# Kernel optimization log

Hardware: AMD Instinct MI355X
Metric: run time of the kernel (lower is better)

Reference implementation:

```python
import jax, jax.numpy as jnp
import numpy as np

N = 100000      # nodes
E = 800000      # edges
F_IN = 128      # input feature dim
HID = 8         # per-head hidden
HEADS = 8
HD = HID * HEADS  # 64
G = 128         # graphs in batch
C = 10          # classes
SLOPE = 0.2     # leaky relu negative slope


def setup_inputs() -> dict:
    key = jax.random.key(0)
    ks = iter(jax.random.split(key, 48))
    def rn(shape, scale=0.1):
        return jax.random.normal(next(ks), shape, jnp.float32) * scale
    inp = {
        'x': jax.random.normal(next(ks), (N, F_IN), jnp.float32),
        'edge_index': jax.random.randint(next(ks), (2, E), 0, N),
        'batch': jnp.sort(jax.random.randint(next(ks), (N,), 0, G)),
        # GAT layer 1
        'W1': rn((F_IN, HEADS * HID)), 'as1': rn((HEADS, HID)), 'ad1': rn((HEADS, HID)), 'b1': jnp.zeros((HEADS * HID,), jnp.float32),
        # GAT layer 2
        'W2': rn((HD, HEADS * HID)), 'as2': rn((HEADS, HID)), 'ad2': rn((HEADS, HID)), 'b2': jnp.zeros((HEADS * HID,), jnp.float32),
        # node attention MLP (HD -> HD//2 -> 2)
        'na_w1': rn((HD, HD // 2)), 'na_b1': jnp.zeros((HD // 2,), jnp.float32), 'na_w2': rn((HD // 2, 2)), 'na_b2': jnp.zeros((2,), jnp.float32),
        # edge attention MLP (2*HD -> HD -> 2)
        'ea_w1': rn((2 * HD, HD)), 'ea_b1': jnp.zeros((HD,), jnp.float32), 'ea_w2': rn((HD, 2)), 'ea_b2': jnp.zeros((2,), jnp.float32),
        # GCN causal / trivial
        'gc_w': rn((HD, HD)), 'gc_b': jnp.zeros((HD,), jnp.float32),
        'gt_w': rn((HD, HD)), 'gt_b': jnp.zeros((HD,), jnp.float32),
        # readouts
        'rc_w': rn((HD, HD)), 'rc_b': jnp.zeros((HD,), jnp.float32),
        'rt_w': rn((HD, HD)), 'rt_b': jnp.zeros((HD,), jnp.float32),
        # classifiers (HD -> HD//2 -> C), combined (2HD -> HD -> C)
        'cc_w1': rn((HD, HD // 2)), 'cc_b1': jnp.zeros((HD // 2,), jnp.float32), 'cc_w2': rn((HD // 2, C)), 'cc_b2': jnp.zeros((C,), jnp.float32),
        'ct_w1': rn((HD, HD // 2)), 'ct_b1': jnp.zeros((HD // 2,), jnp.float32), 'ct_w2': rn((HD // 2, C)), 'ct_b2': jnp.zeros((C,), jnp.float32),
        'cm_w1': rn((2 * HD, HD)), 'cm_b1': jnp.zeros((HD,), jnp.float32), 'cm_w2': rn((HD, C)), 'cm_b2': jnp.zeros((C,), jnp.float32),
    }
    return inp


def _mlp2(h, w1, b1, w2, b2):
    return jax.nn.relu(h @ w1 + b1) @ w2 + b2


def reference(x, edge_index, batch,
              W1, as1, ad1, b1, W2, as2, ad2, b2,
              na_w1, na_b1, na_w2, na_b2,
              ea_w1, ea_b1, ea_w2, ea_b2,
              gc_w, gc_b, gt_w, gt_b,
              rc_w, rc_b, rt_w, rt_b,
              cc_w1, cc_b1, cc_w2, cc_b2,
              ct_w1, ct_b1, ct_w2, ct_b2,
              cm_w1, cm_b1, cm_w2, cm_b2):
    src, dst = edge_index[0], edge_index[1]
    loop = jnp.arange(N)
    s2 = jnp.concatenate([src, loop])  # edges + self-loops (PyG GATConv/GCNConv add self-loops)
    d2 = jnp.concatenate([dst, loop])

    def gat(h_in, W, a_s, a_d, b):
        h = (h_in @ W).reshape(N, HEADS, HID)
        es = jnp.einsum('nhd,hd->nh', h, a_s)
        ed = jnp.einsum('nhd,hd->nh', h, a_d)
        logit = jax.nn.leaky_relu(es[s2] + ed[d2], SLOPE)      # [E+N, H]
        m = jax.ops.segment_max(logit, d2, num_segments=N)
        ex = jnp.exp(logit - m[d2])
        den = jax.ops.segment_sum(ex, d2, num_segments=N)
        alpha = ex / (den[d2] + 1e-16)
        out = jax.ops.segment_sum(h[s2] * alpha[..., None], d2, num_segments=N)
        return out.reshape(N, HEADS * HID) + b

    # GNN encoder (dropout disabled: eval mode)
    H1 = jax.nn.elu(gat(x, W1, as1, ad1, b1))
    H = gat(H1, W2, as2, ad2, b2)                              # [N, HD]

    # node attention
    na = jax.nn.softmax(_mlp2(H, na_w1, na_b1, na_w2, na_b2), axis=1)
    alpha_c, alpha_t = na[:, 0], na[:, 1]
    # edge attention (original edges, no self-loops)
    ef = jnp.concatenate([H[src], H[dst]], axis=1)             # [E, 2*HD]
    ea = jax.nn.softmax(_mlp2(ef, ea_w1, ea_b1, ea_w2, ea_b2), axis=1)
    beta_c, beta_t = ea[:, 0], ea[:, 1]

    Hc = H * alpha_c[:, None]
    Ht = H * alpha_t[:, None]

    def gcn(h_in, w, b, ew):
        # PyG gcn_norm: self-loops with weight 1, symmetric deg^-1/2 normalization
        w_full = jnp.concatenate([ew, jnp.ones((N,), h_in.dtype)])
        deg = jax.ops.segment_sum(w_full, d2, num_segments=N)
        dis = jnp.where(deg > 0, jax.lax.rsqrt(jnp.maximum(deg, 1e-20)), 0.0)
        norm = dis[s2] * w_full * dis[d2]
        h = h_in @ w
        return jax.ops.segment_sum(h[s2] * norm[:, None], d2, num_segments=N) + b

    Gc = gcn(Hc, gc_w, gc_b, beta_c)
    Gt = gcn(Ht, gt_w, gt_b, beta_t)

    # readout: linear then global_add_pool
    hGc = jax.ops.segment_sum(Gc @ rc_w + rc_b, batch, num_segments=G)  # [G, HD]
    hGt = jax.ops.segment_sum(Gt @ rt_w + rt_b, batch, num_segments=G)

    zc = _mlp2(hGc, cc_w1, cc_b1, cc_w2, cc_b2)
    zt = _mlp2(hGt, ct_w1, ct_b1, ct_w2, ct_b2)
    # RandomIntervention: within-graph node shuffle followed by add-pool == plain add-pool
    h_comb = jnp.concatenate([hGc + hGt], axis=1) if False else (hGc + hGt)
    zp = _mlp2(jnp.concatenate([h_comb, jnp.zeros_like(h_comb)], axis=1), cm_w1, cm_b1, cm_w2, cm_b2) if False else _mlp2_comb(h_comb, cm_w1, cm_b1, cm_w2, cm_b2)
    return (zc, zt, zp, hGc, hGt)


def _mlp2_comb(h_comb, cm_w1, cm_b1, cm_w2, cm_b2):
    # original: classifier_combined takes hidden_dim*2 input; forward feeds h_G_c + shuffled_h_G_t
    # which is [G, HD]; to match Linear(2*HD, ...) we use the first HD rows of cm_w1 twice?
    # NO -- the original code as written passes a [G, HD] tensor to a Linear(2*HD, HD) layer,
    # which would error in torch. Faithful runnable interpretation: combined feature is
    # concat([h_G_c, shuffled_h_G_t]) of width 2*HD (the standard CAL formulation).
    return jax.nn.relu(h_comb @ cm_w1 + cm_b1) @ cm_w2 + cm_b2


# clean final definition overriding the commented exploration above
def reference(x, edge_index, batch,
              W1, as1, ad1, b1, W2, as2, ad2, b2,
              na_w1, na_b1, na_w2, na_b2,
              ea_w1, ea_b1, ea_w2, ea_b2,
              gc_w, gc_b, gt_w, gt_b,
              rc_w, rc_b, rt_w, rt_b,
              cc_w1, cc_b1, cc_w2, cc_b2,
              ct_w1, ct_b1, ct_w2, ct_b2,
              cm_w1, cm_b1, cm_w2, cm_b2):
    src, dst = edge_index[0], edge_index[1]
    loop = jnp.arange(N)
    s2 = jnp.concatenate([src, loop])
    d2 = jnp.concatenate([dst, loop])

    def gat(h_in, W, a_s, a_d, b):
        h = (h_in @ W).reshape(N, HEADS, HID)
        es = jnp.einsum('nhd,hd->nh', h, a_s)
        ed = jnp.einsum('nhd,hd->nh', h, a_d)
        logit = jax.nn.leaky_relu(es[s2] + ed[d2], SLOPE)
        m = jax.ops.segment_max(logit, d2, num_segments=N)
        ex = jnp.exp(logit - m[d2])
        den = jax.ops.segment_sum(ex, d2, num_segments=N)
        alpha = ex / (den[d2] + 1e-16)
        out = jax.ops.segment_sum(h[s2] * alpha[..., None], d2, num_segments=N)
        return out.reshape(N, HEADS * HID) + b

    H1 = jax.nn.elu(gat(x, W1, as1, ad1, b1))
    H = gat(H1, W2, as2, ad2, b2)

    na = jax.nn.softmax(_mlp2(H, na_w1, na_b1, na_w2, na_b2), axis=1)
    alpha_c, alpha_t = na[:, 0], na[:, 1]
    ef = jnp.concatenate([H[src], H[dst]], axis=1)
    ea = jax.nn.softmax(_mlp2(ef, ea_w1, ea_b1, ea_w2, ea_b2), axis=1)
    beta_c, beta_t = ea[:, 0], ea[:, 1]

    Hc = H * alpha_c[:, None]
    Ht = H * alpha_t[:, None]

    def gcn(h_in, w, b, ew):
        w_full = jnp.concatenate([ew, jnp.ones((N,), h_in.dtype)])
        deg = jax.ops.segment_sum(w_full, d2, num_segments=N)
        dis = jnp.where(deg > 0, jax.lax.rsqrt(jnp.maximum(deg, 1e-20)), 0.0)
        norm = dis[s2] * w_full * dis[d2]
        h = h_in @ w
        return jax.ops.segment_sum(h[s2] * norm[:, None], d2, num_segments=N) + b

    Gc = gcn(Hc, gc_w, gc_b, beta_c)
    Gt = gcn(Ht, gt_w, gt_b, beta_t)

    hGc = jax.ops.segment_sum(Gc @ rc_w + rc_b, batch, num_segments=G)
    hGt = jax.ops.segment_sum(Gt @ rt_w + rt_b, batch, num_segments=G)

    zc = _mlp2(hGc, cc_w1, cc_b1, cc_w2, cc_b2)
    zt = _mlp2(hGt, ct_w1, ct_b1, ct_w2, ct_b2)
    # RandomIntervention with sorted batch: within-graph permutation + add-pool == add-pool
    h_comb = jnp.concatenate([hGc, hGt], axis=1)  # [G, 2*HD] for Linear(2*HD, ...)
    zp = _mlp2(h_comb, cm_w1, cm_b1, cm_w2, cm_b2)
    return (zc, zt, zp, hGc, hGt)


if __name__ == '__main__':
    out = reference(**setup_inputs())
    print([o.shape for o in out])
```

## Files before the change

kernel.cpp:

```cpp
#include <hip/hip_runtime.h>
#include <hip/hip_bf16.h>

#define N_NODES 100000
#define E_EDGES 800000
#define E2 (E_EDGES + N_NODES)
#define FIN 128
#define HD 64
#define NH 8
#define NG 128
#define NC 10
#define SLOPE 0.2f
#define SELF_FLAG 0x40000000
#define SRC_MASK  0x3FFFFFFF
#define NSCAN_BLK 391
#define NBLK64 1563
#define GB 16

#define U1_STRIPES 261
#define U1_GRID (2 + U1_STRIPES * 7)
#define U1_HISTB (U1_STRIPES * 4)
#define T1 (U1_STRIPES * 3)
#define U2_STRIPES 391
#define U2_GRID (U2_STRIPES * 11)

// ... 65 lines not shown
#pragma unroll 2
        for (int k = 0; k < KH; k += 4) {
            float4 w0 = Wsv[(k + 0) * 16 + tc];
            float4 w1 = Wsv[(k + 1) * 16 + tc];
            float4 w2 = Wsv[(k + 2) * 16 + tc];
            float4 w3 = Wsv[(k + 3) * 16 + tc];
            int kq = (h * KH + k) >> 2;
#pragma unroll
            for (int i = 0; i < 4; ++i) {
                float4 r = R4[(tr * 4 + i) * (RS / 4) + kq];
                acc[i][0] = fmaf(r.x, w0.x, fmaf(r.y, w1.x, fmaf(r.z, w2.x, fmaf(r.w, w3.x, acc[i][0]))));
                acc[i][1] = fmaf(r.x, w0.y, fmaf(r.y, w1.y, fmaf(r.z, w2.y, fmaf(r.w, w3.y, acc[i][1]))));
                acc[i][2] = fmaf(r.x, w0.z, fmaf(r.y, w1.z, fmaf(r.z, w2.z, fmaf(r.w, w3.z, acc[i][2]))));
                acc[i][3] = fmaf(r.x, w0.w, fmaf(r.y, w1.w, fmaf(r.z, w2.w, fmaf(r.w, w3.w, acc[i][3]))));
            }
        }
    }

    int j0 = tc * 4;
#pragma unroll
    for (int i = 0; i < 4; ++i) {
        int n = base + tr * 4 + i;
        if (n < N_NODES) {
            ushort4 ov;
            ov.x = f2bf(acc[i][0]); ov.y = f2bf(acc[i][1]);
            ov.z = f2bf(acc[i][2]); ov.w = f2bf(acc[i][3]);
            *(ushort4*)(outB + (size_t)n * 64 + j0) = ov;
        }
    }
    if (MODE == 1) {
        float s0[4], s1[4];
#pragma unroll
        for (int i = 0; i < 4; ++i) {
            float pes = 0.f, ped = 0.f;
#pragma unroll
            for (int q = 0; q < 4; ++q) {
                pes = fmaf(acc[i][q], a_s[j0 + q], pes);
                ped = fmaf(acc[i][q], a_d[j0 + q], ped);
            }
            pes += __shfl_xor(pes, 1, 64);
            ped += __shfl_xor(ped, 1, 64);
            s0[i] = pes; s1[i] = ped;
        }
        if ((tc & 1) == 0) {
            int h = tc >> 1;
#pragma unroll
            for (int i = 0; i < 4; ++i) {
                int n = base + tr * 4 + i;
                if (n < N_NODES) {
                    es[n * NH + h] = s0[i];
                    ed[n * NH + h] = s1[i];
                }
            }
        }
    }
}

__device__ __forceinline__
void gemm_dual_body(float* smem, int tile,
                    const bfu* __restrict__ in, const float* __restrict__ W0,
                    const float* __restrict__ W1,
                    bfu* __restrict__ out0, bfu* __restrict__ out1)
{
    float* Ws   = smem;
    float* rows = smem + 8192;
    int t = threadIdx.x;
    int base = tile * 64;
    {
        const float4* W0v = (const float4*)W0;
        const float4* W1v = (const float4*)W1;
        float4* Wsv = (float4*)Ws;
        for (int i = t; i < 1024; i += 256) { Wsv[i] = W0v[i]; Wsv[1024 + i] = W1v[i]; }
    }
    for (int i = t; i < 64 * 8; i += 256) {
        int r = i >> 3, c = (i & 7) * 8;
        int n = base + r;
        uint4 v = make_uint4(0, 0, 0, 0);
        if (n < N_NODES) v = *(const uint4*)(in + (size_t)n * 64 + c);
        float* dp = rows + r * 68 + c;
        *(float4*)dp       = make_float4(bflo(v.x), bfhi(v.x), bflo(v.y), bfhi(v.y));
        *(float4*)(dp + 4) = make_float4(bflo(v.z), bfhi(v.z), bflo(v.w), bfhi(v.w));
    }
    __syncthreads();
    int tr = t >> 4, tc = t & 15;
    float a0[4][4] = {}, a1[4][4] = {};
    const float4* Wsv = (const float4*)Ws;
    const float4* R4 = (const float4*)rows;
#pragma unroll 2
    for (int k = 0; k < 64; k += 4) {
        float4 p0 = Wsv[(k + 0) * 16 + tc];
        float4 p1 = Wsv[(k + 1) * 16 + tc];
        float4 p2 = Wsv[(k + 2) * 16 + tc];
        float4 p3 = Wsv[(k + 3) * 16 + tc];
        float4 q0 = Wsv[1024 + (k + 0) * 16 + tc];
        float4 q1 = Wsv[1024 + (k + 1) * 16 + tc];
        float4 q2 = Wsv[1024 + (k + 2) * 16 + tc];
        float4 q3 = Wsv[1024 + (k + 3) * 16 + tc];
        int kq = k >> 2;
#pragma unroll
        for (int i = 0; i < 4; ++i) {
            float4 r = R4[(tr * 4 + i) * 17 + kq];
            a0[i][0] = fmaf(r.x, p0.x, fmaf(r.y, p1.x, fmaf(r.z, p2.x, fmaf(r.w, p3.x, a0[i][0]))));
            a0[i][1] = fmaf(r.x, p0.y, fmaf(r.y, p1.y, fmaf(r.z, p2.y, fmaf(r.w, p3.y, a0[i][1]))));
            a0[i][2] = fmaf(r.x, p0.z, fmaf(r.y, p1.z, fmaf(r.z, p2.z, fmaf(r.w, p3.z, a0[i][2]))));
            a0[i][3] = fmaf(r.x, p0.w, fmaf(r.y, p1.w, fmaf(r.z, p2.w, fmaf(r.w, p3.w, a0[i][3]))));
            a1[i][0] = fmaf(r.x, q0.x, fmaf(r.y, q1.x, fmaf(r.z, q2.x, fmaf(r.w, q3.x, a1[i][0]))));
            a1[i][1] = fmaf(r.x, q0.y, fmaf(r.y, q1.y, fmaf(r.z, q2.y, fmaf(r.w, q3.y, a1[i][1]))));
            a1[i][2] = fmaf(r.x, q0.z, fmaf(r.y, q1.z, fmaf(r.z, q2.z, fmaf(r.w, q3.z, a1[i][2]))));
            a1[i][3] = fmaf(r.x, q0.w, fmaf(r.y, q1.w, fmaf(r.z, q2.w, fmaf(r.w, q3.w, a1[i][3]))));
        }
    }
    int j0 = tc * 4;
#pragma unroll
    for (int i = 0; i < 4; ++i) {
        int n = base + tr * 4 + i;
        if (n >= N_NODES) continue;
        ushort4 o0, o1;
        o0.x = f2bf(a0[i][0]); o0.y = f2bf(a0[i][1]);
        o0.z = f2bf(a0[i][2]); o0.w = f2bf(a0[i][3]);
        o1.x = f2bf(a1[i][0]); o1.y = f2bf(a1[i][1]);
        o1.z = f2bf(a1[i][2]); o1.w = f2bf(a1[i][3]);
        *(ushort4*)(out0 + (size_t)n * 64 + j0) = o0;
        *(ushort4*)(out1 + (size_t)n * 64 + j0) = o1;
    }
}

__device__ __forceinline__
void node_att_body(float* smem, int tile,
                   const bfu* __restrict__ H, const float* __restrict__ w1,
                   const float* __restrict__ b1, const float* __restrict__ w2,
                   const float* __restrict__ b2, float2* __restrict__ al2)
{
    float* w1s  = smem;
    float* w2s  = smem + 2048;
    float* rows = smem + 2112;
    int t = threadIdx.x;
    int base = tile * 64;
    {
        const float4* w1v = (const float4*)w1;
        float4* dst = (float4*)w1s;
        for (int i = t; i < 512; i += 256) dst[i] = w1v[i];
    }
    if (t < 64) w2s[t] = w2[t];
    for (int i = t; i < 64 * 8; i += 256) {
        int r = i >> 3, c = (i & 7) * 8;
        int n = base + r;
        uint4 v = make_uint4(0, 0, 0, 0);
        if (n < N_NODES) v = *(const uint4*)(H + (size_t)n * 64 + c);
        float* dp = rows + r * 65 + c;
        dp[0] = bflo(v.x); dp[1] = bfhi(v.x);
        dp[2] = bflo(v.y); dp[3] = bfhi(v.y);
        dp[4] = bflo(v.z); dp[5] = bfhi(v.z);
        dp[6] = bflo(v.w); dp[7] = bfhi(v.w);
    }
    __syncthreads();
    int tr = t >> 3;
    int tc = t & 7;
    float4 bv = *(const float4*)(b1 + tc * 4);
    float4 acc0 = bv, acc1 = bv;
    const float4* w1sv = (const float4*)w1s;
#pragma unroll 8
    for (int k = 0; k < 64; ++k) {
        float4 w = w1sv[k * 8 + tc];
        float r0 = rows[tr * 65 + k];
        float r1 = rows[(tr + 32) * 65 + k];
        acc0.x = fmaf(r0, w.x, acc0.x); acc0.y = fmaf(r0, w.y, acc0.y);
        acc0.z = fmaf(r0, w.z, acc0.z); acc0.w = fmaf(r0, w.w, acc0.w);
        acc1.x = fmaf(r1, w.x, acc1.x); acc1.y = fmaf(r1, w.y, acc1.y);
        acc1.z = fmaf(r1, w.z, acc1.z); acc1.w = fmaf(r1, w.w, acc1.w);
    }
    float z00 = 0.f, z01 = 0.f, z10 = 0.f, z11 = 0.f;
    float h0, w20, w21;
    int j0 = tc * 4;
#pragma unroll
    for (int q = 0; q < 4; ++q) {
        float a0q = q == 0 ? acc0.x : q == 1 ? acc0.y : q == 2 ? acc0.z : acc0.w;
        float a1q = q == 0 ? acc1.x : q == 1 ? acc1.y : q == 2 ? acc1.z : acc1.w;
        w20 = w2s[(j0 + q) * 2]; w21 = w2s[(j0 + q) * 2 + 1];
        h0 = fmaxf(a0q, 0.f);
        z00 = fmaf(h0, w20, z00); z01 = fmaf(h0, w21, z01);
        h0 = fmaxf(a1q, 0.f);
        z10 = fmaf(h0, w20, z10); z11 = fmaf(h0, w21, z11);
    }
#pragma unroll
    for (int o = 1; o < 8; o <<= 1) {
        z00 += __shfl_xor(z00, o, 64); z01 += __shfl_xor(z01, o, 64);
        z10 += __shfl_xor(z10, o, 64); z11 += __shfl_xor(z11, o, 64);
    }
    if (tc == 0) {
        int n0 = base + tr, n1 = base + tr + 32;
        if (n0 < N_NODES) {
            float zz0 = z00 + b2[0], zz1 = z01 + b2[1];
            float mx = fmaxf(zz0, zz1);
            float e0 = __expf(zz0 - mx), e1 = __expf(zz1 - mx);
            float ss = e0 + e1;
            al2[n0] = make_float2(e0 / ss, e1 / ss);
        }
        if (n1 < N_NODES) {
            float zz0 = z10 + b2[0], zz1 = z11 + b2[1];
            float mx = fmaxf(zz0, zz1);
            float e0 = __expf(zz0 - mx), e1 = __expf(zz1 - mx);
            float ss = e0 + e1;
            al2[n1] = make_float2(e0 / ss, e1 / ss);
        }
    }
}

__device__ __forceinline__
void weight_prep_body(float* smem,
                      const float* __restrict__ gw, const float* __restrict__ gb,
                      const float* __restrict__ rw, const float* __restrict__ rb,
                      float* __restrict__ Wp, float* __restrict__ bp)
{
    float* A = smem;
    float* B = smem + 4096;
    int t = threadIdx.x;
    {
        const float4* ga = (const float4*)gw;
        const float4* rA = (const float4*)rw;
        float4* dA = (float4*)A; float4* dB = (float4*)B;
        for (int i = t; i < 1024; i += 256) { dA[i] = ga[i]; dB[i] = rA[i]; }
    }
    __syncthreads();
    for (int e = t * 16; e < t * 16 + 16; ++e) {
        int k = e >> 6, j = e & 63;
        float acc = 0.f;
#pragma unroll 8
        for (int m = 0; m < 64; ++m) acc = fmaf(A[k * 64 + m], B[m * 64 + j], acc);
        Wp[e] = acc;
    }
    if (t < 64) {
        float acc = rb[t];
#pragma unroll 8
        for (int m = 0; m < 64; ++m) acc = fmaf(gb[m], B[m * 64 + t], acc);
        bp[t] = acc;
    }
}

__global__ __launch_bounds__(256)
void u1_fused(const float* __restrict__ x, const float* __restrict__ W1,
              bfu* __restrict__ B0, const float* __restrict__ as1,
              const float* __restrict__ ad1, float* __restrict__ es,
              float* __restrict__ ed,
              const int* __restrict__ ei, int* __restrict__ cnt,
              int* __restrict__ rank,
              const float* __restrict__ gc_w, const float* __restrict__ gc_b,
              const float* __restrict__ rc_w, const float* __restrict__ rc_b,
              const float* __restrict__ gt_w, const float* __restrict__ gt_b,
              const float* __restrict__ rt_w, const float* __restrict__ rt_b,
              float* __restrict__ Wcp, float* __restrict__ bcp,
              float* __restrict__ Wtp, float* __restrict__ btp)
{
    __shared__ __align__(16) float smem[12544];
    int b = blockIdx.x;
    if (b < 2) {
        if (b == 0) weight_prep_body(smem, gc_w, gc_b, rc_w, rc_b, Wcp, bcp);
        else        weight_prep_body(smem, gt_w, gt_b, rt_w, rt_b, Wtp, btp);
        return;
    }
    int u = b - 2;
    int stripe = u / 7, r = u % 7;
    if (r < 3) {
        gemm_tile_body<float, FIN, 1>(smem, stripe * 3 + r, x, W1, B0, as1, ad1, es, ed);
    } else {
        int idx = stripe * 4 + (r - 3);
        int t = threadIdx.x;
        const int STR = U1_HISTB * 256;
        for (int e = idx * 256 + t; e < E_EDGES; e += 2 * STR) {
            int e1 = e + STR;
            int d0 = ei[E_EDGES + e];
            int r0 = atomicAdd(&cnt[d0], 1);
            int r1 = 0;
            bool has1 = e1 < E_EDGES;
            if (has1) r1 = atomicAdd(&cnt[ei[E_EDGES + e1]], 1);
            rank[e] = r0;
            if (has1) rank[e1] = r1;
        }
    }
}

__global__ __launch_bounds__(256)
void u2_fused(const float* __restrict__ x, const float* __restrict__ W1,
              bfu* __restrict__ B0, const float* __restrict__ as1,
              const float* __restrict__ ad1, float* __restrict__ es,
              float* __restrict__ ed,
              const int* __restrict__ ei, const int* __restrict__ rank,
              const int* __restrict__ offs,
              int* __restrict__ csr, int* __restrict__ csrd)
{
    __shared__ __align__(16) float smem[12544];
    int b = blockIdx.x;
    int stripe = b / 11, r = b % 11;
    int t = threadIdx.x;
    if (r < 8) {
        int e = (stripe * 8 + r) * 256 + t;
        if (e < E_EDGES) {
            int s = ei[e], d = ei[E_EDGES + e];
            csr[offs[d] + rank[e]] = s;
        }
    } else if (r < 10) {
        int tile = T1 + stripe * 2 + (r - 8);
        if (tile < NBLK64)
            gemm_tile_body<float, FIN, 1>(smem, tile, x, W1, B0, as1, ad1, es, ed);
    } else {
        int n = stripe * 256 + t;
        if (n < N_NODES) {
            int pb = offs[n], pe = offs[n + 1];
            for (int p = pb; p < pe; ++p) csrd[p] = n;
            csr[pe - 1] = n | SELF_FLAG;
        }
    }
}

__global__ __launch_bounds__(256)
void u3_fused(const bfu* __restrict__ B2,
              const float* __restrict__ na_w1, const float* __restrict__ na_b1,
              const float* __restrict__ na_w2, const float* __restrict__ na_b2,
              float2* __restrict__ al2,
              const float* __restrict__ ea_w1,
              bfu* __restrict__ P1, bfu* __restrict__ P2)
{
    __shared__ __align__(16) float smem[12544];
    int b = blockIdx.x;
    if (b & 1) node_att_body(smem, b >> 1, B2, na_w1, na_b1, na_w2, na_b2, al2);
    else       gemm_dual_body(smem, b >> 1, B2, ea_w1, ea_w1 + 64 * 64, P1, P2);
}

__global__ __launch_bounds__(256)
void gemm_tile_k64(const bfu* __restrict__ in, const float* __restrict__ W,
                   bfu* __restrict__ outB,
                   const float* __restrict__ a_s, const float* __restrict__ a_d,
                   float* __restrict__ es, float* __restrict__ ed)
{
    __shared__ __align__(16) float smem[64 * 64 + 64 * 68];
    gemm_tile_body<bfu, 64, 1>(smem, blockIdx.x, in, W, outB, a_s, a_d, es, ed);
}

__global__ void csr_scan1(const int* __restrict__ cnt, int* __restrict__ offs,
                          int* __restrict__ bsum, const int* __restrict__ batch,
                          int* __restrict__ glo)
{
    __shared__ int tmp[256];
    int t = threadIdx.x;
    int i = blockIdx.x * 256 + t;
    int v = (i < N_NODES) ? cnt[i] + 1 : 0;
    tmp[t] = v; __syncthreads();
#pragma unroll
    for (int o = 1; o < 256; o <<= 1) {
        int a = (t >= o) ? tmp[t - o] : 0;
        __syncthreads();
        tmp[t] += a;
        __syncthreads();
    }
    if (i < N_NODES) offs[i] = tmp[t] - v;
    if (t == 255) bsum[blockIdx.x] = tmp[255];
    if (blockIdx.x == 0 && t <= NG) {
        int l = 0, r = N_NODES;
        while (l < r) { int m = (l + r) >> 1; if (batch[m] < t) l = m + 1; else r = m; }
        glo[t] = l;
    }
}

__global__ void csr_scan23(int* __restrict__ offs, const int* __restrict__ bsum)
{
    __shared__ int tmp[256];
    int b = blockIdx.x;
    int t = threadIdx.x;
    int s = 0;
    for (int j = t; j < b; j += 256) s += bsum[j];
    tmp[t] = s; __syncthreads();
#pragma unroll
    for (int o = 128; o > 0; o >>= 1) {
        if (t < o) tmp[t] += tmp[t + o];
        __syncthreads();
    }
    int prefix = tmp[0];
    int i = b * 256 + t;
    if (i < N_NODES) offs[i] += prefix;
// ... 25 lines not shown
        float ex0 = __expf(l0);
        float ex1 = __expf(l1);
        den += ex0 + ex1;
        ushort4 ra = *(const ushort4*)(hsrcB + (size_t)s0 * HD + fl * 4);
        ushort4 rb = *(const ushort4*)(hsrcB + (size_t)s1 * HD + fl * 4);
        acc.x = fmaf(bf2f(ra.x), ex0, fmaf(bf2f(rb.x), ex1, acc.x));
        acc.y = fmaf(bf2f(ra.y), ex0, fmaf(bf2f(rb.y), ex1, acc.y));
        acc.z = fmaf(bf2f(ra.z), ex0, fmaf(bf2f(rb.z), ex1, acc.z));
        acc.w = fmaf(bf2f(ra.w), ex0, fmaf(bf2f(rb.w), ex1, acc.w));
    }
    if (p < end) {
        int s = csr[p] & SRC_MASK;
        float l = lrelu(es[s * NH + h] + edv);
        float ex = __expf(l);
        den += ex;
        ushort4 rb = *(const ushort4*)(hsrcB + (size_t)s * HD + fl * 4);
        acc.x = fmaf(bf2f(rb.x), ex, acc.x);
        acc.y = fmaf(bf2f(rb.y), ex, acc.y);
        acc.z = fmaf(bf2f(rb.z), ex, acc.z);
        acc.w = fmaf(bf2f(rb.w), ex, acc.w);
    }
#pragma unroll
    for (int o = 16; o <= 32; o <<= 1) {
        den   += __shfl_xor(den,   o, 64);
        acc.x += __shfl_xor(acc.x, o, 64);
        acc.y += __shfl_xor(acc.y, o, 64);
        acc.z += __shfl_xor(acc.z, o, 64);
        acc.w += __shfl_xor(acc.w, o, 64);
    }
    if (g == 0) {
        float inv = 1.f / (den + 1e-16f);
        float4 bv = *(const float4*)(bias + fl * 4);
        float v0 = acc.x * inv + bv.x;
        float v1 = acc.y * inv + bv.y;
        float v2 = acc.z * inv + bv.z;
        float v3 = acc.w * inv + bv.w;
        if (ELU) {
            v0 = v0 > 0.f ? v0 : (__expf(v0) - 1.f);
            v1 = v1 > 0.f ? v1 : (__expf(v1) - 1.f);
            v2 = v2 > 0.f ? v2 : (__expf(v2) - 1.f);
            v3 = v3 > 0.f ? v3 : (__expf(v3) - 1.f);
        }
        ushort4 ov;
        ov.x = f2bf(v0); ov.y = f2bf(v1); ov.z = f2bf(v2); ov.w = f2bf(v3);
        *(ushort4*)(outB + (size_t)n * HD + fl * 4) = ov;
    }
}

__global__ void edge_att_node(const int* __restrict__ offs, const int* __restrict__ csr,
                              const bfu* __restrict__ P1b, const bfu* __restrict__ P2b,
                              const float* __restrict__ b1, const float* __restrict__ w2,
                              const float* __restrict__ b2,
                              const float2* __restrict__ al2,
                              float2* __restrict__ beta2, float2* __restrict__ dis2,
                              float2* __restrict__ prod2)
{
    int n = blockIdx.x * 4 + (threadIdx.x >> 6);
    int lane = threadIdx.x & 63;
    if (n >= N_NODES) return;
    int slot = lane >> 3, q = lane & 7;
    uint4 U2 = *(const uint4*)(P2b + (size_t)n * 64 + q * 8);
    const float4* pb = (const float4*)(b1 + q * 8);
    const float4* pw = (const float4*)(w2 + q * 16);
    float4 c0 = pb[0], c1 = pb[1];
    float4 w0 = pw[0], w1v = pw[1], w2v = pw[2], w3v = pw[3];
    float wd0 = w0.x - w0.y,   wd1 = w0.z - w0.w;
    float wd2 = w1v.x - w1v.y, wd3 = w1v.z - w1v.w;
    float wd4 = w2v.x - w2v.y, wd5 = w2v.z - w2v.w;
    float wd6 = w3v.x - w3v.y, wd7 = w3v.z - w3v.w;
    float zbd = b2[0] - b2[1];
    float d0 = bflo(U2.x) + c0.x, d1 = bfhi(U2.x) + c0.y;
    float d2 = bflo(U2.y) + c0.z, d3 = bfhi(U2.y) + c0.w;
    float d4 = bflo(U2.z) + c1.x, d5 = bfhi(U2.z) + c1.y;
    float d6 = bflo(U2.w) + c1.z, d7 = bfhi(U2.w) + c1.w;
    int beg = offs[n], endr = offs[n + 1] - 1;
    float dc = 0.f, dt = 0.f;
    for (int p = beg + slot; p < endr; p += 8) {
        int s = csr[p];
        uint4 U1 = *(const uint4*)(P1b + (size_t)s * 64 + q * 8);
        float h0 = fmaxf(bflo(U1.x) + d0, 0.f);
        float h1 = fmaxf(bfhi(U1.x) + d1, 0.f);
        float h2 = fmaxf(bflo(U1.y) + d2, 0.f);
        float h3 = fmaxf(bfhi(U1.y) + d3, 0.f);
        float h4 = fmaxf(bflo(U1.z) + d4, 0.f);
        float h5 = fmaxf(bfhi(U1.z) + d5, 0.f);
        float h6 = fmaxf(bflo(U1.w) + d6, 0.f);
        float h7 = fmaxf(bfhi(U1.w) + d7, 0.f);
        float z = fmaf(h0, wd0, fmaf(h1, wd1, fmaf(h2, wd2, fmaf(h3, wd3,
                  fmaf(h4, wd4, fmaf(h5, wd5, fmaf(h6, wd6, h7 * wd7)))))));
        z += __shfl_xor(z, 1, 64);
        z += __shfl_xor(z, 2, 64);
        z += __shfl_xor(z, 4, 64);
        if (q == 0) {
            z += zbd;
            float e = __expf(-fabsf(z));
            float inv = 1.f / (1.f + e);
            float bx = z >= 0.f ? inv : e * inv;
            float by = z >= 0.f ? e * inv : inv;
            beta2[p] = make_float2(bx, by);
            dc += bx; dt += by;
        }
    }
    dc += __shfl_xor(dc, 8, 64);  dt += __shfl_xor(dt, 8, 64);
    dc += __shfl_xor(dc, 16, 64); dt += __shfl_xor(dt, 16, 64);
    dc += __shfl_xor(dc, 32, 64); dt += __shfl_xor(dt, 32, 64);
    if (lane == 0) {
        dc += 1.f; dt += 1.f;
        float ic = rsqrtf(fmaxf(dc, 1e-20f));
        float it = rsqrtf(fmaxf(dt, 1e-20f));
        dis2[n] = make_float2(ic, it);
        float2 al = al2[n];
        prod2[n] = make_float2(ic * al.x, it * al.y);
    }
}

__global__ __launch_bounds__(256)
void gcn_readout_fused(const int* __restrict__ offs, const int* __restrict__ csr,
                       const int* __restrict__ csrd, const int* __restrict__ glo,
                       const bfu* __restrict__ HB,
                       const float2* __restrict__ beta2, const float2* __restrict__ dis2,
                       const float2* __restrict__ prod2,
                       float* __restrict__ Pc, float* __restrict__ Pt)
{
    int g = blockIdx.x / GB, b = blockIdx.x % GB;
    int t = threadIdx.x;
    int pbeg = offs[glo[g]], pend = offs[glo[g + 1]];
    int total = pend - pbeg;
    int chunk = (total + GB - 1) / GB;
    int start = pbeg + b * chunk;
    int end = start + chunk;
    if (end > pend) end = pend;
    if (start > pend) start = pend;
    int slot = t >> 4, fl = t & 15;
    float4 a1 = make_float4(0.f, 0.f, 0.f, 0.f);
    float4 a2 = make_float4(0.f, 0.f, 0.f, 0.f);
    int p = start + slot;
    for (; p + 48 < end; p += 64) {
#pragma unroll
        for (int j = 0; j < 4; ++j) {
            int pp = p + j * 16;
            int sv = csr[pp];
            int s = sv & SRC_MASK;
            float2 bb = beta2[pp];
            if (sv & SELF_FLAG) { bb.x = 1.f; bb.y = 1.f; }
            float2 pr = prod2[s];
            float2 dv = dis2[csrd[pp]];
            float wc = pr.x * bb.x * dv.x;
            float wt = pr.y * bb.y * dv.y;
            ushort4 r0 = *(const ushort4*)(HB + (size_t)s * HD + fl * 4);
            float f0 = bf2f(r0.x), f1 = bf2f(r0.y), f2 = bf2f(r0.z), f3 = bf2f(r0.w);
            a1.x = fmaf(f0, wc, a1.x); a1.y = fmaf(f1, wc, a1.y);
            a1.z = fmaf(f2, wc, a1.z); a1.w = fmaf(f3, wc, a1.w);
            a2.x = fmaf(f0, wt, a2.x); a2.y = fmaf(f1, wt, a2.y);
            a2.z = fmaf(f2, wt, a2.z); a2.w = fmaf(f3, wt, a2.w);
        }
    }
    for (; p < end; p += 16) {
        int sv = csr[p];
        int s = sv & SRC_MASK;
        float2 bb = beta2[p];
        if (sv & SELF_FLAG) { bb.x = 1.f; bb.y = 1.f; }
        float2 pr = prod2[s];
        float2 dv = dis2[csrd[p]];
        float wc = pr.x * bb.x * dv.x;
        float wt = pr.y * bb.y * dv.y;
        ushort4 r0 = *(const ushort4*)(HB + (size_t)s * HD + fl * 4);
        float f0 = bf2f(r0.x), f1 = bf2f(r0.y), f2 = bf2f(r0.z), f3 = bf2f(r0.w);
        a1.x = fmaf(f0, wc, a1.x); a1.y = fmaf(f1, wc, a1.y);
        a1.z = fmaf(f2, wc, a1.z); a1.w = fmaf(f3, wc, a1.w);
        a2.x = fmaf(f0, wt, a2.x); a2.y = fmaf(f1, wt, a2.y);
        a2.z = fmaf(f2, wt, a2.z); a2.w = fmaf(f3, wt, a2.w);
    }
    __shared__ float redc[16 * 64], redt[16 * 64];
    *(float4*)(redc + slot * 64 + fl * 4) = a1;
    *(float4*)(redt + slot * 64 + fl * 4) = a2;
    __syncthreads();
    if (t < 64) {
        float sc = 0.f, st = 0.f;
#pragma unroll
        for (int s = 0; s < 16; ++s) { sc += redc[s * 64 + t]; st += redt[s * 64 + t]; }
        Pc[(size_t)blockIdx.x * 64 + t] = sc;
        Pt[(size_t)blockIdx.x * 64 + t] = st;
    }
}

__global__ __launch_bounds__(64)
void head_final(const float* __restrict__ Pc, const float* __restrict__ Pt,
                const int* __restrict__ glo,
                const float* __restrict__ Wcp, const float* __restrict__ bcp,
                const float* __restrict__ Wtp, const float* __restrict__ btp,
                const float* __restrict__ cc_w1, const float* __restrict__ cc_b1,
                const float* __restrict__ cc_w2, const float* __restrict__ cc_b2,
                const float* __restrict__ ct_w1, const float* __restrict__ ct_b1,
                const float* __restrict__ ct_w2, const float* __restrict__ ct_b2,
                const float* __restrict__ cm_w1, const float* __restrict__ cm_b1,
                const float* __restrict__ cm_w2, const float* __restrict__ cm_b2,
                float* __restrict__ out)
{
    int g = blockIdx.x;
    int t = threadIdx.x;
    __shared__ float scl[64], stl[64], hgc[64], hgt[64], hid[64];
    float sc = 0.f, st = 0.f;
#pragma unroll
    for (int b = 0; b < GB; ++b) {
        sc += Pc[(size_t)(g * GB + b) * 64 + t];
        st += Pt[(size_t)(g * GB + b) * 64 + t];
    }
    scl[t] = sc; stl[t] = st;
    float c = (float)(glo[g + 1] - glo[g]);
    __syncthreads();
    {
        float a = c * bcp[t], bb = c * btp[t];
#pragma unroll 8
        for (int k = 0; k < 64; ++k) {
            a  = fmaf(scl[k], Wcp[k * 64 + t], a);
            bb = fmaf(stl[k], Wtp[k * 64 + t], bb);
        }
        hgc[t] = a; hgt[t] = bb;
// ... 49 lines not shown

extern "C" void kernel_launch(void* const* d_in, const int* in_sizes, int n_in,
                              void* d_out, int out_size, void* d_ws, size_t ws_size,
                              hipStream_t stream)
{
    const float* x     = (const float*)d_in[0];
    const int*   ei    = (const int*)d_in[1];
    const int*   batch = (const int*)d_in[2];
    const float* W1    = (const float*)d_in[3];
    const float* as1   = (const float*)d_in[4];
    const float* ad1   = (const float*)d_in[5];
    const float* b1    = (const float*)d_in[6];
    const float* W2    = (const float*)d_in[7];
    const float* as2   = (const float*)d_in[8];
    const float* ad2   = (const float*)d_in[9];
    const float* b2    = (const float*)d_in[10];
    const float* na_w1 = (const float*)d_in[11];
    const float* na_b1 = (const float*)d_in[12];
    const float* na_w2 = (const float*)d_in[13];
    const float* na_b2 = (const float*)d_in[14];
    const float* ea_w1 = (const float*)d_in[15];
    const float* ea_b1 = (const float*)d_in[16];
    const float* ea_w2 = (const float*)d_in[17];
    const float* ea_b2 = (const float*)d_in[18];
    const float* gc_w  = (const float*)d_in[19];
    const float* gc_b  = (const float*)d_in[20];
    const float* gt_w  = (const float*)d_in[21];
    const float* gt_b  = (const float*)d_in[22];
    const float* rc_w  = (const float*)d_in[23];
    const float* rc_b  = (const float*)d_in[24];
    const float* rt_w  = (const float*)d_in[25];
    const float* rt_b  = (const float*)d_in[26];
    const float* cc_w1 = (const float*)d_in[27];
    const float* cc_b1 = (const float*)d_in[28];
    const float* cc_w2 = (const float*)d_in[29];
    const float* cc_b2 = (const float*)d_in[30];
    const float* ct_w1 = (const float*)d_in[31];
    const float* ct_b1 = (const float*)d_in[32];
    const float* ct_w2 = (const float*)d_in[33];
    const float* ct_b2 = (const float*)d_in[34];
    const float* cm_w1 = (const float*)d_in[35];
    const float* cm_b1 = (const float*)d_in[36];
    const float* cm_w2 = (const float*)d_in[37];
    const float* cm_b2 = (const float*)d_in[38];
    float* out = (float*)d_out;

    float* ws = (float*)d_ws;
    size_t o = 0;
    const size_t nf = (size_t)N_NODES * HD;
    float* es    = ws + o; o += (size_t)N_NODES * NH;
    float* ed    = ws + o; o += (size_t)N_NODES * NH;
    float2* al2  = (float2*)(ws + o); o += (size_t)N_NODES * 2;
    float2* beta2= (float2*)(ws + o); o += (size_t)E2 * 2;
    float2* dis2 = (float2*)(ws + o); o += (size_t)N_NODES * 2;
    float2* prod2= (float2*)(ws + o); o += (size_t)N_NODES * 2;
    bfu* B0      = (bfu*)(ws + o); o += nf / 2;
    bfu* B1      = (bfu*)(ws + o); o += nf / 2;
    bfu* B2      = (bfu*)(ws + o); o += nf / 2;
    bfu* BH1     = (bfu*)(ws + o); o += nf / 2;
    int* csr     = (int*)(ws + o); o += E2;
    int* csrd    = (int*)(ws + o); o += E2;
    int* offs    = (int*)(ws + o); o += N_NODES + 1;
    float* Pc    = ws + o; o += (size_t)NG * GB * 64;
    float* Pt    = ws + o; o += (size_t)NG * GB * 64;
    float* Wcp   = ws + o; o += 4096;
    float* Wtp   = ws + o; o += 4096;
    float* bcp   = ws + o; o += 64;
    float* btp   = ws + o; o += 64;
    int* glo     = (int*)(ws + o); o += NG + 2;
    int* cnt  = (int*)beta2;
    int* bsum = (int*)dis2;
    int* rank = (int*)B1;

    const int NW_BLKS = N_NODES / 4;

    hipMemsetAsync(cnt, 0, (size_t)N_NODES * 4, stream);
    u1_fused<<<U1_GRID, 256, 0, stream>>>(x, W1, B0, as1, ad1, es, ed,
                                          ei, cnt, rank,
                                          gc_w, gc_b, rc_w, rc_b,
                                          gt_w, gt_b, rt_w, rt_b,
                                          Wcp, bcp, Wtp, btp);
    csr_scan1<<<NSCAN_BLK, 256, 0, stream>>>(cnt, offs, bsum, batch, glo);
    csr_scan23<<<NSCAN_BLK, 256, 0, stream>>>(offs, bsum);

    u2_fused<<<U2_GRID, 256, 0, stream>>>(x, W1, B0, as1, ad1, es, ed,
                                          ei, rank, offs, csr, csrd);

    gat_aggregate4<1><<<NW_BLKS, 256, 0, stream>>>(offs, csr, es, ed, B0, b1, BH1);

    gemm_tile_k64<<<NBLK64, 256, 0, stream>>>(BH1, W2, B0, as2, ad2, es, ed);
    gat_aggregate4<0><<<NW_BLKS, 256, 0, stream>>>(offs, csr, es, ed, B0, b2, B2);

    u3_fused<<<2 * NBLK64, 256, 0, stream>>>(B2, na_w1, na_b1, na_w2, na_b2, al2,
                                             ea_w1, B0, B1);

    edge_att_node<<<NW_BLKS, 256, 0, stream>>>(offs, csr, B0, B1,
                                               ea_b1, ea_w2, ea_b2, al2,
                                               beta2, dis2, prod2);

    gcn_readout_fused<<<NG * GB, 256, 0, stream>>>(offs, csr, csrd, glo, B2,
                                                   beta2, dis2, prod2, Pc, Pt);

    head_final<<<NG, 64, 0, stream>>>(Pc, Pt, glo,
                                      Wcp, bcp, Wtp, btp,
                                      cc_w1, cc_b1, cc_w2, cc_b2,
                                      ct_w1, ct_b1, ct_w2, ct_b2,
                                      cm_w1, cm_b1, cm_w2, cm_b2, out);
    (void)in_sizes; (void)n_in; (void)out_size; (void)ws_size;
}
```

Before: 479.2 us.

## Fold destination degree norm into edge weights and drop csrd array

```diff
diff --git a/kernel.cpp b/kernel.cpp
--- a/kernel.cpp
+++ b/kernel.cpp
@@ -141,156 +141,6 @@
                     ed[n * NH + h] = s1[i];
                 }
             }
-        }
-    }
-}
-
-__device__ __forceinline__
-void gemm_dual_body(float* smem, int tile,
-                    const bfu* __restrict__ in, const float* __restrict__ W0,
-                    const float* __restrict__ W1,
-                    bfu* __restrict__ out0, bfu* __restrict__ out1)
-{
-    float* Ws   = smem;
-    float* rows = smem + 8192;
-    int t = threadIdx.x;
-    int base = tile * 64;
-    {
-        const float4* W0v = (const float4*)W0;
-        const float4* W1v = (const float4*)W1;
-        float4* Wsv = (float4*)Ws;
-        for (int i = t; i < 1024; i += 256) { Wsv[i] = W0v[i]; Wsv[1024 + i] = W1v[i]; }
-    }
-    for (int i = t; i < 64 * 8; i += 256) {
-        int r = i >> 3, c = (i & 7) * 8;
-        int n = base + r;
-        uint4 v = make_uint4(0, 0, 0, 0);
-        if (n < N_NODES) v = *(const uint4*)(in + (size_t)n * 64 + c);
-        float* dp = rows + r * 68 + c;
-        *(float4*)dp       = make_float4(bflo(v.x), bfhi(v.x), bflo(v.y), bfhi(v.y));
-        *(float4*)(dp + 4) = make_float4(bflo(v.z), bfhi(v.z), bflo(v.w), bfhi(v.w));
-    }
-    __syncthreads();
-    int tr = t >> 4, tc = t & 15;
-    float a0[4][4] = {}, a1[4][4] = {};
-    const float4* Wsv = (const float4*)Ws;
-    const float4* R4 = (const float4*)rows;
-#pragma unroll 2
-    for (int k = 0; k < 64; k += 4) {
-        float4 p0 = Wsv[(k + 0) * 16 + tc];
-        float4 p1 = Wsv[(k + 1) * 16 + tc];
-        float4 p2 = Wsv[(k + 2) * 16 + tc];
-        float4 p3 = Wsv[(k + 3) * 16 + tc];
-        float4 q0 = Wsv[1024 + (k + 0) * 16 + tc];
-        float4 q1 = Wsv[1024 + (k + 1) * 16 + tc];
-        float4 q2 = Wsv[1024 + (k + 2) * 16 + tc];
-        float4 q3 = Wsv[1024 + (k + 3) * 16 + tc];
-        int kq = k >> 2;
-#pragma unroll
-        for (int i = 0; i < 4; ++i) {
-            float4 r = R4[(tr * 4 + i) * 17 + kq];
-            a0[i][0] = fmaf(r.x, p0.x, fmaf(r.y, p1.x, fmaf(r.z, p2.x, fmaf(r.w, p3.x, a0[i][0]))));
-            a0[i][1] = fmaf(r.x, p0.y, fmaf(r.y, p1.y, fmaf(r.z, p2.y, fmaf(r.w, p3.y, a0[i][1]))));
-            a0[i][2] = fmaf(r.x, p0.z, fmaf(r.y, p1.z, fmaf(r.z, p2.z, fmaf(r.w, p3.z, a0[i][2]))));
-            a0[i][3] = fmaf(r.x, p0.w, fmaf(r.y, p1.w, fmaf(r.z, p2.w, fmaf(r.w, p3.w, a0[i][3]))));
-            a1[i][0] = fmaf(r.x, q0.x, fmaf(r.y, q1.x, fmaf(r.z, q2.x, fmaf(r.w, q3.x, a1[i][0]))));
-            a1[i][1] = fmaf(r.x, q0.y, fmaf(r.y, q1.y, fmaf(r.z, q2.y, fmaf(r.w, q3.y, a1[i][1]))));
-            a1[i][2] = fmaf(r.x, q0.z, fmaf(r.y, q1.z, fmaf(r.z, q2.z, fmaf(r.w, q3.z, a1[i][2]))));
-            a1[i][3] = fmaf(r.x, q0.w, fmaf(r.y, q1.w, fmaf(r.z, q2.w, fmaf(r.w, q3.w, a1[i][3]))));
-        }
-    }
-    int j0 = tc * 4;
-#pragma unroll
-    for (int i = 0; i < 4; ++i) {
-        int n = base + tr * 4 + i;
-        if (n >= N_NODES) continue;
-        ushort4 o0, o1;
-        o0.x = f2bf(a0[i][0]); o0.y = f2bf(a0[i][1]);
-        o0.z = f2bf(a0[i][2]); o0.w = f2bf(a0[i][3]);
-        o1.x = f2bf(a1[i][0]); o1.y = f2bf(a1[i][1]);
-        o1.z = f2bf(a1[i][2]); o1.w = f2bf(a1[i][3]);
-        *(ushort4*)(out0 + (size_t)n * 64 + j0) = o0;
-        *(ushort4*)(out1 + (size_t)n * 64 + j0) = o1;
-    }
-}
-
-__device__ __forceinline__
-void node_att_body(float* smem, int tile,
-                   const bfu* __restrict__ H, const float* __restrict__ w1,
-                   const float* __restrict__ b1, const float* __restrict__ w2,
-                   const float* __restrict__ b2, float2* __restrict__ al2)
-{
-    float* w1s  = smem;
-    float* w2s  = smem + 2048;
-    float* rows = smem + 2112;
-    int t = threadIdx.x;
-    int base = tile * 64;
-    {
-        const float4* w1v = (const float4*)w1;
-        float4* dst = (float4*)w1s;
-        for (int i = t; i < 512; i += 256) dst[i] = w1v[i];
-    }
-    if (t < 64) w2s[t] = w2[t];
-    for (int i = t; i < 64 * 8; i += 256) {
-        int r = i >> 3, c = (i & 7) * 8;
-        int n = base + r;
-        uint4 v = make_uint4(0, 0, 0, 0);
-        if (n < N_NODES) v = *(const uint4*)(H + (size_t)n * 64 + c);
-        float* dp = rows + r * 65 + c;
-        dp[0] = bflo(v.x); dp[1] = bfhi(v.x);
-        dp[2] = bflo(v.y); dp[3] = bfhi(v.y);
-        dp[4] = bflo(v.z); dp[5] = bfhi(v.z);
-        dp[6] = bflo(v.w); dp[7] = bfhi(v.w);
-    }
-    __syncthreads();
-    int tr = t >> 3;
-    int tc = t & 7;
-    float4 bv = *(const float4*)(b1 + tc * 4);
-    float4 acc0 = bv, acc1 = bv;
-    const float4* w1sv = (const float4*)w1s;
-#pragma unroll 8
-    for (int k = 0; k < 64; ++k) {
-        float4 w = w1sv[k * 8 + tc];
-        float r0 = rows[tr * 65 + k];
-        float r1 = rows[(tr + 32) * 65 + k];
-        acc0.x = fmaf(r0, w.x, acc0.x); acc0.y = fmaf(r0, w.y, acc0.y);
-        acc0.z = fmaf(r0, w.z, acc0.z); acc0.w = fmaf(r0, w.w, acc0.w);
-        acc1.x = fmaf(r1, w.x, acc1.x); acc1.y = fmaf(r1, w.y, acc1.y);
-        acc1.z = fmaf(r1, w.z, acc1.z); acc1.w = fmaf(r1, w.w, acc1.w);
-    }
-    float z00 = 0.f, z01 = 0.f, z10 = 0.f, z11 = 0.f;
-    float h0, w20, w21;
-    int j0 = tc * 4;
-#pragma unroll
-    for (int q = 0; q < 4; ++q) {
-        float a0q = q == 0 ? acc0.x : q == 1 ? acc0.y : q == 2 ? acc0.z : acc0.w;
-        float a1q = q == 0 ? acc1.x : q == 1 ? acc1.y : q == 2 ? acc1.z : acc1.w;
-        w20 = w2s[(j0 + q) * 2]; w21 = w2s[(j0 + q) * 2 + 1];
-        h0 = fmaxf(a0q, 0.f);
-        z00 = fmaf(h0, w20, z00); z01 = fmaf(h0, w21, z01);
-        h0 = fmaxf(a1q, 0.f);
-        z10 = fmaf(h0, w20, z10); z11 = fmaf(h0, w21, z11);
-    }
-#pragma unroll
-    for (int o = 1; o < 8; o <<= 1) {
-        z00 += __shfl_xor(z00, o, 64); z01 += __shfl_xor(z01, o, 64);
-        z10 += __shfl_xor(z10, o, 64); z11 += __shfl_xor(z11, o, 64);
-    }
-    if (tc == 0) {
-        int n0 = base + tr, n1 = base + tr + 32;
-        if (n0 < N_NODES) {
-            float zz0 = z00 + b2[0], zz1 = z01 + b2[1];
-            float mx = fmaxf(zz0, zz1);
-            float e0 = __expf(zz0 - mx), e1 = __expf(zz1 - mx);
-            float ss = e0 + e1;
-            al2[n0] = make_float2(e0 / ss, e1 / ss);
-        }
-        if (n1 < N_NODES) {
-            float zz0 = z10 + b2[0], zz1 = z11 + b2[1];
-            float mx = fmaxf(zz0, zz1);
-            float e0 = __expf(zz0 - mx), e1 = __expf(zz1 - mx);
-            float ss = e0 + e1;
-            al2[n1] = make_float2(e0 / ss, e1 / ss);
         }
     }
 }
@@ -375,7 +225,7 @@
               float* __restrict__ ed,
               const int* __restrict__ ei, const int* __restrict__ rank,
               const int* __restrict__ offs,
-              int* __restrict__ csr, int* __restrict__ csrd)
+              int* __restrict__ csr)
 {
     __shared__ __align__(16) float smem[12544];
     int b = blockIdx.x;
@@ -394,25 +244,145 @@
     } else {
         int n = stripe * 256 + t;
         if (n < N_NODES) {
-            int pb = offs[n], pe = offs[n + 1];
-            for (int p = pb; p < pe; ++p) csrd[p] = n;
-            csr[pe - 1] = n | SELF_FLAG;
+            csr[offs[n + 1] - 1] = n | SELF_FLAG;
         }
     }
 }
 
 __global__ __launch_bounds__(256)
-void u3_fused(const bfu* __restrict__ B2,
+void u3_fused(const bfu* __restrict__ in,
               const float* __restrict__ na_w1, const float* __restrict__ na_b1,
               const float* __restrict__ na_w2, const float* __restrict__ na_b2,
               float2* __restrict__ al2,
               const float* __restrict__ ea_w1,
-              bfu* __restrict__ P1, bfu* __restrict__ P2)
+              bfu* __restrict__ out0, bfu* __restrict__ out1)
 {
     __shared__ __align__(16) float smem[12544];
-    int b = blockIdx.x;
-    if (b & 1) node_att_body(smem, b >> 1, B2, na_w1, na_b1, na_w2, na_b2, al2);
-    else       gemm_dual_body(smem, b >> 1, B2, ea_w1, ea_w1 + 64 * 64, P1, P2);
+    float* Ws   = smem;
+    float* rows = smem + 8192;
+    int t = threadIdx.x;
+    int base = blockIdx.x * 64;
+    const float* W0 = ea_w1;
+    const float* W1 = ea_w1 + 64 * 64;
+    {
+        const float4* W0v = (const float4*)W0;
+        const float4* W1v = (const float4*)W1;
+        float4* Wsv = (float4*)Ws;
+        for (int i = t; i < 1024; i += 256) { Wsv[i] = W0v[i]; Wsv[1024 + i] = W1v[i]; }
+    }
+    for (int i = t; i < 64 * 8; i += 256) {
+        int r = i >> 3, c = (i & 7) * 8;
+        int n = base + r;
+        uint4 v = make_uint4(0, 0, 0, 0);
+        if (n < N_NODES) v = *(const uint4*)(in + (size_t)n * 64 + c);
+        float* dp = rows + r * 68 + c;
+        *(float4*)dp       = make_float4(bflo(v.x), bfhi(v.x), bflo(v.y), bfhi(v.y));
+        *(float4*)(dp + 4) = make_float4(bflo(v.z), bfhi(v.z), bflo(v.w), bfhi(v.w));
+    }
+    __syncthreads();
+    {
+        int tr = t >> 4, tc = t & 15;
+        float a0[4][4] = {}, a1[4][4] = {};
+        const float4* Wsv = (const float4*)Ws;
+        const float4* R4 = (const float4*)rows;
+#pragma unroll 2
+        for (int k = 0; k < 64; k += 4) {
+            float4 p0 = Wsv[(k + 0) * 16 + tc];
+            float4 p1 = Wsv[(k + 1) * 16 + tc];
+            float4 p2 = Wsv[(k + 2) * 16 + tc];
+            float4 p3 = Wsv[(k + 3) * 16 + tc];
+            float4 q0 = Wsv[1024 + (k + 0) * 16 + tc];
+            float4 q1 = Wsv[1024 + (k + 1) * 16 + tc];
+            float4 q2 = Wsv[1024 + (k + 2) * 16 + tc];
+            float4 q3 = Wsv[1024 + (k + 3) * 16 + tc];
+            int kq = k >> 2;
+#pragma unroll
+            for (int i = 0; i < 4; ++i) {
+                float4 r = R4[(tr * 4 + i) * 17 + kq];
+                a0[i][0] = fmaf(r.x, p0.x, fmaf(r.y, p1.x, fmaf(r.z, p2.x, fmaf(r.w, p3.x, a0[i][0]))));
+                a0[i][1] = fmaf(r.x, p0.y, fmaf(r.y, p1.y, fmaf(r.z, p2.y, fmaf(r.w, p3.y, a0[i][1]))));
+                a0[i][2] = fmaf(r.x, p0.z, fmaf(r.y, p1.z, fmaf(r.z, p2.z, fmaf(r.w, p3.z, a0[i][2]))));
+                a0[i][3] = fmaf(r.x, p0.w, fmaf(r.y, p1.w, fmaf(r.z, p2.w, fmaf(r.w, p3.w, a0[i][3]))));
+                a1[i][0] = fmaf(r.x, q0.x, fmaf(r.y, q1.x, fmaf(r.z, q2.x, fmaf(r.w, q3.x, a1[i][0]))));
+                a1[i][1] = fmaf(r.x, q0.y, fmaf(r.y, q1.y, fmaf(r.z, q2.y, fmaf(r.w, q3.y, a1[i][1]))));
+                a1[i][2] = fmaf(r.x, q0.z, fmaf(r.y, q1.z, fmaf(r.z, q2.z, fmaf(r.w, q3.z, a1[i][2]))));
+                a1[i][3] = fmaf(r.x, q0.w, fmaf(r.y, q1.w, fmaf(r.z, q2.w, fmaf(r.w, q3.w, a1[i][3]))));
+            }
+        }
+        int j0 = tc * 4;
+#pragma unroll
+        for (int i = 0; i < 4; ++i) {
+            int n = base + tr * 4 + i;
+            if (n >= N_NODES) continue;
+            ushort4 o0, o1;
+            o0.x = f2bf(a0[i][0]); o0.y = f2bf(a0[i][1]);
+            o0.z = f2bf(a0[i][2]); o0.w = f2bf(a0[i][3]);
+            o1.x = f2bf(a1[i][0]); o1.y = f2bf(a1[i][1]);
+            o1.z = f2bf(a1[i][2]); o1.w = f2bf(a1[i][3]);
+            *(ushort4*)(out0 + (size_t)n * 64 + j0) = o0;
+            *(ushort4*)(out1 + (size_t)n * 64 + j0) = o1;
+        }
+    }
+    __syncthreads();
+    {
+        const float4* w1v = (const float4*)na_w1;
+        float4* dst = (float4*)Ws;
+        for (int i = t; i < 512; i += 256) dst[i] = w1v[i];
+        if (t < 64) Ws[2048 + t] = na_w2[t];
+    }
+    __syncthreads();
+    {
+        int tr = t >> 3;
+        int tc = t & 7;
+        float4 bv = *(const float4*)(na_b1 + tc * 4);
+        float4 acc0 = bv, acc1 = bv;
+        const float4* w1sv = (const float4*)Ws;
+#pragma unroll 8
+        for (int k = 0; k < 64; ++k) {
+            float4 w = w1sv[k * 8 + tc];
+            float r0 = rows[tr * 68 + k];
+            float r1 = rows[(tr + 32) * 68 + k];
+            acc0.x = fmaf(r0, w.x, acc0.x); acc0.y = fmaf(r0, w.y, acc0.y);
+            acc0.z = fmaf(r0, w.z, acc0.z); acc0.w = fmaf(r0, w.w, acc0.w);
+            acc1.x = fmaf(r1, w.x, acc1.x); acc1.y = fmaf(r1, w.y, acc1.y);
+            acc1.z = fmaf(r1, w.z, acc1.z); acc1.w = fmaf(r1, w.w, acc1.w);
+        }
+        float z00 = 0.f, z01 = 0.f, z10 = 0.f, z11 = 0.f;
+        float h0, w20, w21;
+        int j0 = tc * 4;
+#pragma unroll
+        for (int q = 0; q < 4; ++q) {
+            float a0q = q == 0 ? acc0.x : q == 1 ? acc0.y : q == 2 ? acc0.z : acc0.w;
+            float a1q = q == 0 ? acc1.x : q == 1 ? acc1.y : q == 2 ? acc1.z : acc1.w;
+            w20 = Ws[2048 + (j0 + q) * 2]; w21 = Ws[2048 + (j0 + q) * 2 + 1];
+            h0 = fmaxf(a0q, 0.f);
+            z00 = fmaf(h0, w20, z00); z01 = fmaf(h0, w21, z01);
+            h0 = fmaxf(a1q, 0.f);
+            z10 = fmaf(h0, w20, z10); z11 = fmaf(h0, w21, z11);
+        }
+#pragma unroll
+        for (int o = 1; o < 8; o <<= 1) {
+            z00 += __shfl_xor(z00, o, 64); z01 += __shfl_xor(z01, o, 64);
+            z10 += __shfl_xor(z10, o, 64); z11 += __shfl_xor(z11, o, 64);
+        }
+        if (tc == 0) {
+            int n0 = base + tr, n1 = base + tr + 32;
+            if (n0 < N_NODES) {
+                float zz0 = z00 + na_b2[0], zz1 = z01 + na_b2[1];
+                float mx = fmaxf(zz0, zz1);
+                float e0 = __expf(zz0 - mx), e1 = __expf(zz1 - mx);
+                float ss = e0 + e1;
+                al2[n0] = make_float2(e0 / ss, e1 / ss);
+            }
+            if (n1 < N_NODES) {
+                float zz0 = z10 + na_b2[0], zz1 = z11 + na_b2[1];
+                float mx = fmaxf(zz0, zz1);
+                float e0 = __expf(zz0 - mx), e1 = __expf(zz1 - mx);
+                float ss = e0 + e1;
+                al2[n1] = make_float2(e0 / ss, e1 / ss);
+            }
+        }
+    }
 }
 
 __global__ __launch_bounds__(256)
@@ -544,7 +514,7 @@
                               const float* __restrict__ b1, const float* __restrict__ w2,
                               const float* __restrict__ b2,
                               const float2* __restrict__ al2,
-                              float2* __restrict__ beta2, float2* __restrict__ dis2,
+                              float2* __restrict__ beta2,
                               float2* __restrict__ prod2)
 {
     int n = blockIdx.x * 4 + (threadIdx.x >> 6);
@@ -596,21 +566,27 @@
     dc += __shfl_xor(dc, 8, 64);  dt += __shfl_xor(dt, 8, 64);
     dc += __shfl_xor(dc, 16, 64); dt += __shfl_xor(dt, 16, 64);
     dc += __shfl_xor(dc, 32, 64); dt += __shfl_xor(dt, 32, 64);
+    dc = __shfl(dc, 0, 64); dt = __shfl(dt, 0, 64);
+    dc += 1.f; dt += 1.f;
+    float ic = rsqrtf(fmaxf(dc, 1e-20f));
+    float it = rsqrtf(fmaxf(dt, 1e-20f));
     if (lane == 0) {
-        dc += 1.f; dt += 1.f;
-        float ic = rsqrtf(fmaxf(dc, 1e-20f));
-        float it = rsqrtf(fmaxf(dt, 1e-20f));
-        dis2[n] = make_float2(ic, it);
         float2 al = al2[n];
         prod2[n] = make_float2(ic * al.x, it * al.y);
     }
+    asm volatile("s_waitcnt vmcnt(0)" ::: "memory");
+    for (int p = beg + lane; p < endr; p += 64) {
+        float2 v = beta2[p];
+        beta2[p] = make_float2(v.x * ic, v.y * it);
+    }
+    if (lane == 0) beta2[endr] = make_float2(ic, it);
 }
 
 __global__ __launch_bounds__(256)
 void gcn_readout_fused(const int* __restrict__ offs, const int* __restrict__ csr,
-                       const int* __restrict__ csrd, const int* __restrict__ glo,
+                       const int* __restrict__ glo,
                        const bfu* __restrict__ HB,
-                       const float2* __restrict__ beta2, const float2* __restrict__ dis2,
+                       const float2* __restrict__ beta2,
                        const float2* __restrict__ prod2,
                        float* __restrict__ Pc, float* __restrict__ Pt)
 {
@@ -631,14 +607,11 @@
 #pragma unroll
         for (int j = 0; j < 4; ++j) {
             int pp = p + j * 16;
-            int sv = csr[pp];
-            int s = sv & SRC_MASK;
+            int s = csr[pp] & SRC_MASK;
             float2 bb = beta2[pp];
-            if (sv & SELF_FLAG) { bb.x = 1.f; bb.y = 1.f; }
             float2 pr = prod2[s];
-            float2 dv = dis2[csrd[pp]];
-            float wc = pr.x * bb.x * dv.x;
-            float wt = pr.y * bb.y * dv.y;
+            float wc = pr.x * bb.x;
+            float wt = pr.y * bb.y;
             ushort4 r0 = *(const ushort4*)(HB + (size_t)s * HD + fl * 4);
             float f0 = bf2f(r0.x), f1 = bf2f(r0.y), f2 = bf2f(r0.z), f3 = bf2f(r0.w);
             a1.x = fmaf(f0, wc, a1.x); a1.y = fmaf(f1, wc, a1.y);
@@ -648,14 +621,11 @@
         }
     }
     for (; p < end; p += 16) {
-        int sv = csr[p];
-        int s = sv & SRC_MASK;
+        int s = csr[p] & SRC_MASK;
         float2 bb = beta2[p];
-        if (sv & SELF_FLAG) { bb.x = 1.f; bb.y = 1.f; }
         float2 pr = prod2[s];
-        float2 dv = dis2[csrd[p]];
-        float wc = pr.x * bb.x * dv.x;
-        float wt = pr.y * bb.y * dv.y;
+        float wc = pr.x * bb.x;
+        float wt = pr.y * bb.y;
         ushort4 r0 = *(const ushort4*)(HB + (size_t)s * HD + fl * 4);
         float f0 = bf2f(r0.x), f1 = bf2f(r0.y), f2 = bf2f(r0.z), f3 = bf2f(r0.w);
         a1.x = fmaf(f0, wc, a1.x); a1.y = fmaf(f1, wc, a1.y);
@@ -811,14 +781,12 @@
     float* ed    = ws + o; o += (size_t)N_NODES * NH;
     float2* al2  = (float2*)(ws + o); o += (size_t)N_NODES * 2;
     float2* beta2= (float2*)(ws + o); o += (size_t)E2 * 2;
-    float2* dis2 = (float2*)(ws + o); o += (size_t)N_NODES * 2;
     float2* prod2= (float2*)(ws + o); o += (size_t)N_NODES * 2;
     bfu* B0      = (bfu*)(ws + o); o += nf / 2;
     bfu* B1      = (bfu*)(ws + o); o += nf / 2;
     bfu* B2      = (bfu*)(ws + o); o += nf / 2;
     bfu* BH1     = (bfu*)(ws + o); o += nf / 2;
     int* csr     = (int*)(ws + o); o += E2;
-    int* csrd    = (int*)(ws + o); o += E2;
     int* offs    = (int*)(ws + o); o += N_NODES + 1;
     float* Pc    = ws + o; o += (size_t)NG * GB * 64;
     float* Pt    = ws + o; o += (size_t)NG * GB * 64;
@@ -828,7 +796,7 @@
     float* btp   = ws + o; o += 64;
     int* glo     = (int*)(ws + o); o += NG + 2;
     int* cnt  = (int*)beta2;
-    int* bsum = (int*)dis2;
+    int* bsum = (int*)prod2;
     int* rank = (int*)B1;
 
     const int NW_BLKS = N_NODES / 4;
@@ -843,22 +811,22 @@
     csr_scan23<<<NSCAN_BLK, 256, 0, stream>>>(offs, bsum);
 
     u2_fused<<<U2_GRID, 256, 0, stream>>>(x, W1, B0, as1, ad1, es, ed,
-                                          ei, rank, offs, csr, csrd);
+                                          ei, rank, offs, csr);
 
     gat_aggregate4<1><<<NW_BLKS, 256, 0, stream>>>(offs, csr, es, ed, B0, b1, BH1);
 
     gemm_tile_k64<<<NBLK64, 256, 0, stream>>>(BH1, W2, B0, as2, ad2, es, ed);
     gat_aggregate4<0><<<NW_BLKS, 256, 0, stream>>>(offs, csr, es, ed, B0, b2, B2);
 
-    u3_fused<<<2 * NBLK64, 256, 0, stream>>>(B2, na_w1, na_b1, na_w2, na_b2, al2,
-                                             ea_w1, B0, B1);
+    u3_fused<<<NBLK64, 256, 0, stream>>>(B2, na_w1, na_b1, na_w2, na_b2, al2,
+                                         ea_w1, B0, B1);
 
     edge_att_node<<<NW_BLKS, 256, 0, stream>>>(offs, csr, B0, B1,
                                                ea_b1, ea_w2, ea_b2, al2,
-                                               beta2, dis2, prod2);
-
-    gcn_readout_fused<<<NG * GB, 256, 0, stream>>>(offs, csr, csrd, glo, B2,
-                                                   beta2, dis2, prod2, Pc, Pt);
+                                               beta2, prod2);
+
+    gcn_readout_fused<<<NG * GB, 256, 0, stream>>>(offs, csr, glo, B2,
+                                                   beta2, prod2, Pc, Pt);
 
     head_final<<<NG, 64, 0, stream>>>(Pc, Pt, glo,
                                       Wcp, bcp, Wtp, btp,
```

New measurement: 474.3 us. About the same (-1.0%).
